# Kernel optimization log

Hardware: AMD Instinct MI355X
Metric: run time of the kernel (lower is better)

The kernel has to match this reference:

```python
import jax, jax.numpy as jnp
import numpy as np

B, S, D = 2, 2048, 1024
H = 16
HD = D // H  # 64


def setup_inputs() -> dict:
    key = jax.random.key(0)
    k1, k2, k3, k4, k5, k6 = jax.random.split(key, 6)
    hidden_states = jax.random.normal(k1, (B, S, D), dtype=jnp.float32)
    attention_mask = jax.random.randint(k2, (B, S), 0, 2, dtype=jnp.int32)
    scale = 1.0 / np.sqrt(D)
    Wq = jax.random.normal(k3, (D, D), dtype=jnp.float32) * scale
    bq = jax.random.normal(k4, (D,), dtype=jnp.float32) * 0.02
    Wk = jax.random.normal(k5, (D, D), dtype=jnp.float32) * scale
    bk = jax.random.normal(k6, (D,), dtype=jnp.float32) * 0.02
    return {"hidden_states": hidden_states, "attention_mask": attention_mask,
            "Wq": Wq, "bq": bq, "Wk": Wk, "bk": bk}


def _split_heads(x):
    # [B, S, D] -> [B, H, S, HD]
    b, s, _ = x.shape
    return x.reshape(b, s, H, HD).transpose(0, 2, 1, 3)


def reference(hidden_states, attention_mask, Wq, bq, Wk, bk):
    dh = jnp.sqrt(jnp.float32(HD))
    q = _split_heads(hidden_states @ Wq + bq)            # [B,H,S,HD]
    k = _split_heads(hidden_states @ Wk + bk)            # [B,H,S,HD]
    v = q + k                                            # value = Q + K
    k_t = -jax.nn.log_sigmoid(-k)                        # negate the logsigmoid(-K) transform
    scores = jnp.einsum('bhqd,bhkd->bhqk', q, k_t) / dh  # [B,H,S,S]
    # mask applied on the QUERY axis (dim 2), broadcast over key axis (faithful to source)
    mask = (attention_mask[:, None, :, None] == 0)       # [B,1,S,1]
    scores = jnp.where(mask, jnp.float32(-10000.0), scores)
    probs = jax.nn.softmax(scores, axis=-1)              # dropout: eval mode (identity)
    ctx = jnp.einsum('bhqk,bhkd->bhqd', probs, v)        # [B,H,S,HD]
    ctx = ctx.transpose(0, 2, 1, 3).reshape(B, S, D)
    return ctx
```

## Files before the change

### kernel.cpp

```cpp
#include <hip/hip_runtime.h>
#include <hip/hip_bf16.h>

#define B_ 2
#define S_ 2048
#define D_ 1024
#define H_ 16
#define HD_ 64

typedef __attribute__((ext_vector_type(8))) short short8;
typedef __attribute__((ext_vector_type(4))) short short4v;
typedef __attribute__((ext_vector_type(4))) float float4v;

typedef const __attribute__((address_space(1))) void* gas_ptr;
typedef __attribute__((address_space(3))) void* las_ptr;

static __device__ inline void gl_lds16(const void* g, void* l) {
  __builtin_amdgcn_global_load_lds((gas_ptr)g, (las_ptr)l, 16, 0, 0);
}

static __device__ inline short f2bs(float x) {
  __hip_bfloat16 h = __float2bfloat16(x);
  union { __hip_bfloat16 h; short s; } u; u.h = h; return u.s;
}
static __device__ inline float bs2f(short s) {
  union { short s; __hip_bfloat16 h; } u; u.s = s; return __bfloat162float(u.h);
}
static __device__ inline short4v pk4(float a, float b, float c, float d) {
  union { __hip_bfloat162 h[2]; short4v s; } u;
  u.h[0] = __float22bfloat162_rn(float2{a, b});
  u.h[1] = __float22bfloat162_rn(float2{c, d});
  return u.s;
}

static __device__ inline float4v mfma32(short8 a, short8 b, float4v c) {
  return __builtin_amdgcn_mfma_f32_16x16x32_bf16(a, b, c, 0, 0, 0);
}
static __device__ inline float4v mfma16(short4v a, short4v b, float4v c) {
  return __builtin_amdgcn_mfma_f32_16x16x16bf16_1k(a, b, c, 0, 0, 0);
}

__global__ __launch_bounds__(256) void prep(
    const float* __restrict__ hs, __hip_bfloat16* __restrict__ hsb,
    const float* __restrict__ Wq, const float* __restrict__ Wk,
    __hip_bfloat16* __restrict__ Wqt, __hip_bfloat16* __restrict__ Wkt) {
  __shared__ float t[64][65];
  const int id = blockIdx.x;
  if (id < 2048) {
    const size_t i = ((size_t)id * 256 + threadIdx.x) * 8;
    const float4v a0 = ((const float4v*)(hs + i))[0];
    const float4v a1 = ((const float4v*)(hs + i))[1];
    short8 s;
#pragma unroll
    for (int j = 0; j < 4; ++j) { s[j] = f2bs(a0[j]); s[4 + j] = f2bs(a1[j]); }
    *(short8*)(hsb + i) = s;
    return;
  }
  const int bid = id - 2048;
  const float* W = (bid >> 8) ? Wk : Wq;
  __hip_bfloat16* Wt = (bid >> 8) ? Wkt : Wqt;
  const int n0 = (bid & 15) * 64, k0 = ((bid >> 4) & 15) * 64;
  const int c = threadIdx.x & 63, r0 = threadIdx.x >> 6;
  for (int i = 0; i < 16; ++i) {
    const int r = i * 4 + r0;
    t[c][r] = W[(size_t)(k0 + r) * D_ + n0 + c];
  }
  __syncthreads();
  for (int i = 0; i < 16; ++i) {
    const int rr = i * 4 + r0;
    Wt[(size_t)(n0 + rr) * D_ + k0 + c] = __float2bfloat16(t[rr][c]);
  }
}

__global__ __launch_bounds__(256, 2) void gemm_fused(
    const __hip_bfloat16* __restrict__ hsb,
    const __hip_bfloat16* __restrict__ Wqt, const __hip_bfloat16* __restrict__ Wkt,
    const float* __restrict__ bq, const float* __restrict__ bk,
    __hip_bfloat16* __restrict__ q_out, __hip_bfloat16* __restrict__ kt_out,
    __hip_bfloat16* __restrict__ vT) {
  const int id = blockIdx.x;
  const int mt = (id & 7) * 8 + ((id >> 3) & 7);
  const int nt = id >> 6;
  const int n0 = nt * 128, m0 = mt * 64;
  __shared__ __hip_bfloat16 As[2][64 * 32];
  __shared__ __hip_bfloat16 Bq[2][128 * 32];
  __shared__ __hip_bfloat16 Bk[2][128 * 32];
  const int tid = threadIdx.x, wid = tid >> 6, lane = tid & 63;
  const int wm = (wid >> 1) * 32, wn = (wid & 1) * 64;
  const int l15 = lane & 15, l4 = lane >> 4;
  const float4v zz = {0.f, 0.f, 0.f, 0.f};
  float4v accq[2][4], acck[2][4];
  for (int i = 0; i < 2; ++i)
    for (int j = 0; j < 4; ++j) { accq[i][j] = zz; acck[i][j] = zz; }
  const int lrow = wid * 16 + (lane >> 2);
  const int lk8 = (((lane & 3) ^ ((lane >> 3) & 3)) * 8);
  {
    gl_lds16(hsb + (size_t)(m0 + lrow) * D_ + lk8, As[0] + wid * 512);
    gl_lds16(Wqt + (size_t)(n0 + lrow) * D_ + lk8, Bq[0] + wid * 512);
    gl_lds16(Wqt + (size_t)(n0 + 64 + lrow) * D_ + lk8, Bq[0] + 2048 + wid * 512);
    gl_lds16(Wkt + (size_t)(n0 + lrow) * D_ + lk8, Bk[0] + wid * 512);
    gl_lds16(Wkt + (size_t)(n0 + 64 + lrow) * D_ + lk8, Bk[0] + 2048 + wid * 512);
  }
  int p = 0;
  for (int kb = 0; kb < 32; ++kb) {
    __syncthreads();
    if (kb < 31) {
      const int kc = (kb + 1) * 32 + lk8;
      gl_lds16(hsb + (size_t)(m0 + lrow) * D_ + kc, As[p ^ 1] + wid * 512);
      gl_lds16(Wqt + (size_t)(n0 + lrow) * D_ + kc, Bq[p ^ 1] + wid * 512);
      gl_lds16(Wqt + (size_t)(n0 + 64 + lrow) * D_ + kc, Bq[p ^ 1] + 2048 + wid * 512);
      gl_lds16(Wkt + (size_t)(n0 + lrow) * D_ + kc, Bk[p ^ 1] + wid * 512);
      gl_lds16(Wkt + (size_t)(n0 + 64 + lrow) * D_ + kc, Bk[p ^ 1] + 2048 + wid * 512);
    }
    short8 af[2], bfq[4], bfk[4];
    const int fo = ((l4 ^ ((l15 >> 1) & 3)) * 8);
    for (int rt = 0; rt < 2; ++rt)
      af[rt] = *(const short8*)(As[p] + (wm + rt * 16 + l15) * 32 + fo);
    for (int ct = 0; ct < 4; ++ct) {
      bfq[ct] = *(const short8*)(Bq[p] + (wn + ct * 16 + l15) * 32 + fo);
      bfk[ct] = *(const short8*)(Bk[p] + (wn + ct * 16 + l15) * 32 + fo);
    }
    for (int rt = 0; rt < 2; ++rt)
      for (int ct = 0; ct < 4; ++ct) {
        accq[rt][ct] = mfma32(af[rt], bfq[ct], accq[rt][ct]);
        acck[rt][ct] = mfma32(af[rt], bfk[ct], acck[rt][ct]);
      }
    p ^= 1;
  }
  float bvq[4], bvk[4];
  for (int ct = 0; ct < 4; ++ct) {
    bvq[ct] = bq[n0 + wn + ct * 16 + l15];
    bvk[ct] = bk[n0 + wn + ct * 16 + l15];
  }
  for (int rt = 0; rt < 2; ++rt)
    for (int ct = 0; ct < 4; ++ct) {
      const int col = n0 + wn + ct * 16 + l15;
      const int h = col >> 6, d = col & 63;
      const int rowb = m0 + wm + rt * 16 + l4 * 4;
      short4v vv;
      for (int r = 0; r < 4; ++r) {
        const int row = rowb + r;
        const float qv = accq[rt][ct][r] + bvq[ct];
        const float kv = acck[rt][ct][r] + bvk[ct];
        const float sp = fmaxf(kv, 0.f) + __logf(1.f + __expf(-fabsf(kv)));
        q_out[(size_t)row * D_ + col] = __float2bfloat16(qv);
        kt_out[(size_t)row * D_ + col] = __float2bfloat16(sp);
        vv[r] = f2bs(qv + kv);
      }
      const int b = rowb >> 11, s = rowb & 2047;
      const int sw = (s & ~63) | (((s >> 4) & 3) << 2) | (((s >> 2) & 3) << 4);
      *(short4v*)(vT + ((size_t)(b * H_ + h) * HD_ + d) * S_ + sw) = vv;
    }
}

__global__ __launch_bounds__(256, 2) void attn(
    const __hip_bfloat16* __restrict__ qb, const __hip_bfloat16* __restrict__ ktb,
    const __hip_bfloat16* __restrict__ vT, const int* __restrict__ mask,
    float* __restrict__ out) {
  __shared__ short smem[32768];
  const int id = blockIdx.x;
  const int xcd = id & 7;
  const int rest = id >> 3;
  const int q0 = (rest & 15) * 128;
  const int hb = (rest >> 4) * 8 + xcd;
  const int h = hb >> 1, b = hb & 1;
  const int tid = threadIdx.x, wid = tid >> 6, lane = tid & 63;
  const int l15 = lane & 15, l4 = lane >> 4;
  const __hip_bfloat16* qh = qb + (size_t)b * S_ * D_ + h * HD_;
  const __hip_bfloat16* kh = ktb + (size_t)b * S_ * D_ + h * HD_;
  const __hip_bfloat16* vh = vT + (size_t)(b * H_ + h) * HD_ * S_;
  const int srow = tid >> 2;
  const int b0 = tid & 3;
  const int ssw = ((srow & 1) << 2) | ((srow >> 1) & 3);
  const int w0 = srow * 64 + ((b0 ^ ssw) * 8);
  const int w1 = srow * 64 + (((b0 + 4) ^ ssw) * 8);

  const int qlA = wid * 32 + l15, qlB = qlA + 16;
  const int qrA = q0 + qlA, qrB = q0 + qlB;
  const float SC = 0.125f * 1.44269504f;
  const float mqA = (mask[b * S_ + qrA] != 0) ? SC : 0.f;
  const float mqB = (mask[b * S_ + qrB] != 0) ? SC : 0.f;
  const short8 rA0 = *(const short8*)(qh + (size_t)qrA * D_ + l4 * 8);
  const short8 rA1 = *(const short8*)(qh + (size_t)qrA * D_ + 32 + l4 * 8);
  const short8 rB0 = *(const short8*)(qh + (size_t)qrB * D_ + l4 * 8);
  const short8 rB1 = *(const short8*)(qh + (size_t)qrB * D_ + 32 + l4 * 8);
  short8 bqA0, bqA1, bqB0, bqB1;
  for (int j = 0; j < 8; ++j) {
    bqA0[j] = f2bs(bs2f(rA0[j]) * mqA);
    bqA1[j] = f2bs(bs2f(rA1[j]) * mqA);
    bqB0[j] = f2bs(bs2f(rB0[j]) * mqB);
    bqB1[j] = f2bs(bs2f(rB1[j]) * mqB);
  }

  const int lsw = ((l15 & 1) << 2) | ((l15 >> 1) & 3);
  const int ak0off = l15 * 64 + ((l4 ^ lsw) * 8);
  const int ak1off = l15 * 64 + (((l4 + 4) ^ lsw) * 8);
  const int vb0off = ((2 * l4) ^ lsw) * 8;
  const int vb1off = ((2 * l4 + 1) ^ lsw) * 8;

  const float4v zz = {0.f, 0.f, 0.f, 0.f};
  float4v oaccA[4] = {zz, zz, zz, zz};
  float4v oaccB[4] = {zz, zz, zz, zz};
  float lsumA = 0.f, lsumB = 0.f;

  short8 gk0[2], gk1[2], gv0[2], gv1[2];
#pragma unroll
  for (int u = 0; u < 2; ++u) {
    gk0[u] = *(const short8*)(kh + (size_t)(u * 64 + srow) * D_ + b0 * 8);
    gk1[u] = *(const short8*)(kh + (size_t)(u * 64 + srow) * D_ + b0 * 8 + 32);
    gv0[u] = *(const short8*)(vh + (size_t)srow * S_ + u * 64 + b0 * 8);
    gv1[u] = *(const short8*)(vh + (size_t)srow * S_ + u * 64 + b0 * 8 + 32);
  }

  int p = 0;
  for (int c = 0; c < 16; ++c) {
    short* bufp = smem + p * 16384;
#pragma unroll
    for (int u = 0; u < 2; ++u) {
      *(short8*)(bufp + u * 4096 + w0) = gk0[u];
      *(short8*)(bufp + u * 4096 + w1) = gk1[u];
      *(short8*)(bufp + 8192 + u * 4096 + w0) = gv0[u];
      *(short8*)(bufp + 8192 + u * 4096 + w1) = gv1[u];
    }
    __syncthreads();
    if (c < 15) {
      const int kb = (c + 1) * 128;
#pragma unroll
      for (int u = 0; u < 2; ++u) {
        gk0[u] = *(const short8*)(kh + (size_t)(kb + u * 64 + srow) * D_ + b0 * 8);
        gk1[u] = *(const short8*)(kh + (size_t)(kb + u * 64 + srow) * D_ + b0 * 8 + 32);
        gv0[u] = *(const short8*)(vh + (size_t)srow * S_ + kb + u * 64 + b0 * 8);
        gv1[u] = *(const short8*)(vh + (size_t)srow * S_ + kb + u * 64 + b0 * 8 + 32);
      }
    }
#pragma unroll
    for (int u = 0; u < 2; ++u) {
      const short* kbase = bufp + u * 4096;
      const short* vbase = bufp + 8192 + u * 4096;
      short4v pA[4], pB[4];
#pragma unroll
      for (int t = 0; t < 4; ++t) {
        const short8 ak0 = *(const short8*)(kbase + t * 1024 + ak0off);
        const short8 ak1 = *(const short8*)(kbase + t * 1024 + ak1off);
        float4v cA = zz, cB = zz;
        cA = mfma32(ak0, bqA0, cA);
        cA = mfma32(ak1, bqA1, cA);
        cB = mfma32(ak0, bqB0, cB);
        cB = mfma32(ak1, bqB1, cB);
        float eA[4], eB[4];
#pragma unroll
        for (int r = 0; r < 4; ++r) {
          eA[r] = __builtin_amdgcn_exp2f(cA[r]); lsumA += eA[r];
          eB[r] = __builtin_amdgcn_exp2f(cB[r]); lsumB += eB[r];
        }
        pA[t] = pk4(eA[0], eA[1], eA[2], eA[3]);
        pB[t] = pk4(eB[0], eB[1], eB[2], eB[3]);
      }
#pragma unroll
      for (int dt = 0; dt < 4; ++dt) {
        const int rb = (dt * 16 + l15) * 64;
        const short8 av0 = *(const short8*)(vbase + rb + vb0off);
        const short8 av1 = *(const short8*)(vbase + rb + vb1off);
        const short4v a0 = {av0[0], av0[1], av0[2], av0[3]};
        const short4v a1 = {av0[4], av0[5], av0[6], av0[7]};
        const short4v a2 = {av1[0], av1[1], av1[2], av1[3]};
        const short4v a3 = {av1[4], av1[5], av1[6], av1[7]};
        oaccA[dt] = mfma16(a0, pA[0], oaccA[dt]);
        oaccB[dt] = mfma16(a0, pB[0], oaccB[dt]);
        oaccA[dt] = mfma16(a1, pA[1], oaccA[dt]);
        oaccB[dt] = mfma16(a1, pB[1], oaccB[dt]);
        oaccA[dt] = mfma16(a2, pA[2], oaccA[dt]);
        oaccB[dt] = mfma16(a2, pB[2], oaccB[dt]);
        oaccA[dt] = mfma16(a3, pA[3], oaccA[dt]);
        oaccB[dt] = mfma16(a3, pB[3], oaccB[dt]);
      }
    }
    p ^= 1;
  }
  float lA = lsumA + __shfl_xor(lsumA, 16); lA += __shfl_xor(lA, 32);
  float lB = lsumB + __shfl_xor(lsumB, 16); lB += __shfl_xor(lB, 32);
  __syncthreads();
  float* mbuf = (float*)smem;
  float* mlb = (float*)smem + 128 * 68;
#pragma unroll
  for (int dt = 0; dt < 4; ++dt)
#pragma unroll
    for (int r = 0; r < 4; ++r) {
      mbuf[qlA * 68 + dt * 16 + l4 * 4 + r] = oaccA[dt][r];
      mbuf[qlB * 68 + dt * 16 + l4 * 4 + r] = oaccB[dt][r];
    }
  if (l4 == 0) { mlb[qlA] = lA; mlb[qlB] = lB; }
  __syncthreads();
  const int qq = tid >> 1;
  const int dg = (tid & 1) * 32;
  const float li = 1.f / mlb[qq];
  float* orow = out + (size_t)(b * S_ + q0 + qq) * D_ + h * HD_ + dg;
#pragma unroll
  for (int i = 0; i < 8; ++i) {
    float4v v = *(const float4v*)&mbuf[qq * 68 + dg + i * 4];
#pragma unroll
    for (int r = 0; r < 4; ++r) v[r] *= li;
    *(float4v*)(orow + i * 4) = v;
  }
}

extern "C" void kernel_launch(void* const* d_in, const int* in_sizes, int n_in,
                              void* d_out, int out_size, void* d_ws, size_t ws_size,
                              hipStream_t stream) {
  const float* hs = (const float*)d_in[0];
  const int* mask = (const int*)d_in[1];
  const float* Wq = (const float*)d_in[2];
  const float* bq = (const float*)d_in[3];
  const float* Wk = (const float*)d_in[4];
  const float* bk = (const float*)d_in[5];
  float* out = (float*)d_out;
  char* ws = (char*)d_ws;
  const size_t MB = 1u << 20;
  __hip_bfloat16* q_b = (__hip_bfloat16*)(ws + 0 * MB);
  __hip_bfloat16* k_b = (__hip_bfloat16*)(ws + 8 * MB);
  __hip_bfloat16* vT  = (__hip_bfloat16*)(ws + 16 * MB);
  __hip_bfloat16* Wqt = (__hip_bfloat16*)(ws + 24 * MB);
  __hip_bfloat16* Wkt = (__hip_bfloat16*)(ws + 26 * MB);
  __hip_bfloat16* hsb = (__hip_bfloat16*)(ws + 28 * MB);

  prep<<<dim3(2560), 256, 0, stream>>>(hs, hsb, Wq, Wk, Wqt, Wkt);
  gemm_fused<<<dim3(512), 256, 0, stream>>>(hsb, Wqt, Wkt, bq, bk, q_b, k_b, vT);
  attn<<<dim3(512), 256, 0, stream>>>(q_b, k_b, vT, mask, out);
}
```

Before: 158.6 us.

## Double GEMM K-tile depth to 64 and vectorize attention epilogue stores

```diff
diff --git a/kernel.cpp b/kernel.cpp
--- a/kernel.cpp
+++ b/kernel.cpp
@@ -81,9 +81,9 @@
   const int mt = (id & 7) * 8 + ((id >> 3) & 7);
   const int nt = id >> 6;
   const int n0 = nt * 128, m0 = mt * 64;
-  __shared__ __hip_bfloat16 As[2][64 * 32];
-  __shared__ __hip_bfloat16 Bq[2][128 * 32];
-  __shared__ __hip_bfloat16 Bk[2][128 * 32];
+  __shared__ __hip_bfloat16 As[2][64 * 64];
+  __shared__ __hip_bfloat16 Bq[2][128 * 64];
+  __shared__ __hip_bfloat16 Bk[2][128 * 64];
   const int tid = threadIdx.x, wid = tid >> 6, lane = tid & 63;
   const int wm = (wid >> 1) * 32, wn = (wid & 1) * 64;
   const int l15 = lane & 15, l4 = lane >> 4;
@@ -91,41 +91,52 @@
   float4v accq[2][4], acck[2][4];
   for (int i = 0; i < 2; ++i)
     for (int j = 0; j < 4; ++j) { accq[i][j] = zz; acck[i][j] = zz; }
-  const int lrow = wid * 16 + (lane >> 2);
-  const int lk8 = (((lane & 3) ^ ((lane >> 3) & 3)) * 8);
-  {
-    gl_lds16(hsb + (size_t)(m0 + lrow) * D_ + lk8, As[0] + wid * 512);
-    gl_lds16(Wqt + (size_t)(n0 + lrow) * D_ + lk8, Bq[0] + wid * 512);
-    gl_lds16(Wqt + (size_t)(n0 + 64 + lrow) * D_ + lk8, Bq[0] + 2048 + wid * 512);
-    gl_lds16(Wkt + (size_t)(n0 + lrow) * D_ + lk8, Bk[0] + wid * 512);
-    gl_lds16(Wkt + (size_t)(n0 + 64 + lrow) * D_ + lk8, Bk[0] + 2048 + wid * 512);
-  }
+  const int srow8 = lane >> 3;
+  const int schunk = ((lane & 7) ^ (srow8 & 7)) * 8;
+  const int arow = wid * 16 + srow8;
+  const int brow = wid * 32 + srow8;
+#define STAGE(pp, kc)                                                          \
+  {                                                                            \
+    _Pragma("unroll")                                                          \
+    for (int j = 0; j < 2; ++j)                                                \
+      gl_lds16(hsb + (size_t)(m0 + arow + j * 8) * D_ + (kc) + schunk,         \
+               As[pp] + wid * 1024 + j * 512);                                 \
+    _Pragma("unroll")                                                          \
+    for (int j = 0; j < 4; ++j) {                                              \
+      gl_lds16(Wqt + (size_t)(n0 + brow + j * 8) * D_ + (kc) + schunk,         \
+               Bq[pp] + wid * 2048 + j * 512);                                 \
+      gl_lds16(Wkt + (size_t)(n0 + brow + j * 8) * D_ + (kc) + schunk,         \
+               Bk[pp] + wid * 2048 + j * 512);                                 \
+    }                                                                          \
+  }
+  STAGE(0, 0);
   int p = 0;
-  for (int kb = 0; kb < 32; ++kb) {
+  for (int kb = 0; kb < 16; ++kb) {
     __syncthreads();
-    if (kb < 31) {
-      const int kc = (kb + 1) * 32 + lk8;
-      gl_lds16(hsb + (size_t)(m0 + lrow) * D_ + kc, As[p ^ 1] + wid * 512);
-      gl_lds16(Wqt + (size_t)(n0 + lrow) * D_ + kc, Bq[p ^ 1] + wid * 512);
-      gl_lds16(Wqt + (size_t)(n0 + 64 + lrow) * D_ + kc, Bq[p ^ 1] + 2048 + wid * 512);
-      gl_lds16(Wkt + (size_t)(n0 + lrow) * D_ + kc, Bk[p ^ 1] + wid * 512);
-      gl_lds16(Wkt + (size_t)(n0 + 64 + lrow) * D_ + kc, Bk[p ^ 1] + 2048 + wid * 512);
-    }
-    short8 af[2], bfq[4], bfk[4];
-    const int fo = ((l4 ^ ((l15 >> 1) & 3)) * 8);
-    for (int rt = 0; rt < 2; ++rt)
-      af[rt] = *(const short8*)(As[p] + (wm + rt * 16 + l15) * 32 + fo);
-    for (int ct = 0; ct < 4; ++ct) {
-      bfq[ct] = *(const short8*)(Bq[p] + (wn + ct * 16 + l15) * 32 + fo);
-      bfk[ct] = *(const short8*)(Bk[p] + (wn + ct * 16 + l15) * 32 + fo);
-    }
-    for (int rt = 0; rt < 2; ++rt)
+    if (kb < 15) STAGE(p ^ 1, (kb + 1) * 64);
+#pragma unroll
+    for (int sub = 0; sub < 2; ++sub) {
+      short8 af[2], bfq[4], bfk[4];
+      const int fo = ((sub * 4 + l4) ^ (l15 & 7)) * 8;
+#pragma unroll
+      for (int rt = 0; rt < 2; ++rt)
+        af[rt] = *(const short8*)(As[p] + (wm + rt * 16 + l15) * 64 + fo);
+#pragma unroll
       for (int ct = 0; ct < 4; ++ct) {
-        accq[rt][ct] = mfma32(af[rt], bfq[ct], accq[rt][ct]);
-        acck[rt][ct] = mfma32(af[rt], bfk[ct], acck[rt][ct]);
-      }
+        bfq[ct] = *(const short8*)(Bq[p] + (wn + ct * 16 + l15) * 64 + fo);
+        bfk[ct] = *(const short8*)(Bk[p] + (wn + ct * 16 + l15) * 64 + fo);
+      }
+#pragma unroll
+      for (int rt = 0; rt < 2; ++rt)
+#pragma unroll
+        for (int ct = 0; ct < 4; ++ct) {
+          accq[rt][ct] = mfma32(af[rt], bfq[ct], accq[rt][ct]);
+          acck[rt][ct] = mfma32(af[rt], bfk[ct], acck[rt][ct]);
+        }
+    }
     p ^= 1;
   }
+#undef STAGE
   float bvq[4], bvk[4];
   for (int ct = 0; ct < 4; ++ct) {
     bvq[ct] = bq[n0 + wn + ct * 16 + l15];
@@ -200,7 +211,7 @@
   const float4v zz = {0.f, 0.f, 0.f, 0.f};
   float4v oaccA[4] = {zz, zz, zz, zz};
   float4v oaccB[4] = {zz, zz, zz, zz};
-  float lsumA = 0.f, lsumB = 0.f;
+  float4v lsA = zz, lsB = zz;
 
   short8 gk0[2], gk1[2], gv0[2], gv1[2];
 #pragma unroll
@@ -249,8 +260,8 @@
         float eA[4], eB[4];
 #pragma unroll
         for (int r = 0; r < 4; ++r) {
-          eA[r] = __builtin_amdgcn_exp2f(cA[r]); lsumA += eA[r];
-          eB[r] = __builtin_amdgcn_exp2f(cB[r]); lsumB += eB[r];
+          eA[r] = __builtin_amdgcn_exp2f(cA[r]); lsA[r] += eA[r];
+          eB[r] = __builtin_amdgcn_exp2f(cB[r]); lsB[r] += eB[r];
         }
         pA[t] = pk4(eA[0], eA[1], eA[2], eA[3]);
         pB[t] = pk4(eB[0], eB[1], eB[2], eB[3]);
@@ -276,22 +287,22 @@
     }
     p ^= 1;
   }
-  float lA = lsumA + __shfl_xor(lsumA, 16); lA += __shfl_xor(lA, 32);
-  float lB = lsumB + __shfl_xor(lsumB, 16); lB += __shfl_xor(lB, 32);
+  float lA = (lsA[0] + lsA[1]) + (lsA[2] + lsA[3]);
+  float lB = (lsB[0] + lsB[1]) + (lsB[2] + lsB[3]);
+  lA += __shfl_xor(lA, 16); lA += __shfl_xor(lA, 32);
+  lB += __shfl_xor(lB, 16); lB += __shfl_xor(lB, 32);
   __syncthreads();
   float* mbuf = (float*)smem;
   float* mlb = (float*)smem + 128 * 68;
 #pragma unroll
-  for (int dt = 0; dt < 4; ++dt)
-#pragma unroll
-    for (int r = 0; r < 4; ++r) {
-      mbuf[qlA * 68 + dt * 16 + l4 * 4 + r] = oaccA[dt][r];
-      mbuf[qlB * 68 + dt * 16 + l4 * 4 + r] = oaccB[dt][r];
-    }
+  for (int dt = 0; dt < 4; ++dt) {
+    *(float4v*)&mbuf[qlA * 68 + dt * 16 + l4 * 4] = oaccA[dt];
+    *(float4v*)&mbuf[qlB * 68 + dt * 16 + l4 * 4] = oaccB[dt];
+  }
   if (l4 == 0) { mlb[qlA] = lA; mlb[qlB] = lB; }
   __syncthreads();
-  const int qq = tid >> 1;
-  const int dg = (tid & 1) * 32;
+  const int qq = tid & 127;
+  const int dg = (tid >> 7) * 32;
   const float li = 1.f / mlb[qq];
   float* orow = out + (size_t)(b * S_ + q0 + qq) * D_ + h * HD_ + dg;
 #pragma unroll
```

New measurement: 160.2 us. No clear change (+1.0%).

## Split attention work across waves by query half and key half, reduce in LDS

Applied to the files above, without the earlier changes.

```diff
diff --git a/kernel.cpp b/kernel.cpp
--- a/kernel.cpp
+++ b/kernel.cpp
@@ -165,8 +165,10 @@
   const int h = hb >> 1, b = hb & 1;
   const int tid = threadIdx.x, wid = tid >> 6, lane = tid & 63;
   const int l15 = lane & 15, l4 = lane >> 4;
+  const int qs = (wid & 1) * 64;
+  const int kh = wid >> 1;
   const __hip_bfloat16* qh = qb + (size_t)b * S_ * D_ + h * HD_;
-  const __hip_bfloat16* kh = ktb + (size_t)b * S_ * D_ + h * HD_;
+  const __hip_bfloat16* kh_ = ktb + (size_t)b * S_ * D_ + h * HD_;
   const __hip_bfloat16* vh = vT + (size_t)(b * H_ + h) * HD_ * S_;
   const int srow = tid >> 2;
   const int b0 = tid & 3;
@@ -174,21 +176,19 @@
   const int w0 = srow * 64 + ((b0 ^ ssw) * 8);
   const int w1 = srow * 64 + (((b0 + 4) ^ ssw) * 8);
 
-  const int qlA = wid * 32 + l15, qlB = qlA + 16;
-  const int qrA = q0 + qlA, qrB = q0 + qlB;
   const float SC = 0.125f * 1.44269504f;
-  const float mqA = (mask[b * S_ + qrA] != 0) ? SC : 0.f;
-  const float mqB = (mask[b * S_ + qrB] != 0) ? SC : 0.f;
-  const short8 rA0 = *(const short8*)(qh + (size_t)qrA * D_ + l4 * 8);
-  const short8 rA1 = *(const short8*)(qh + (size_t)qrA * D_ + 32 + l4 * 8);
-  const short8 rB0 = *(const short8*)(qh + (size_t)qrB * D_ + l4 * 8);
-  const short8 rB1 = *(const short8*)(qh + (size_t)qrB * D_ + 32 + l4 * 8);
-  short8 bqA0, bqA1, bqB0, bqB1;
-  for (int j = 0; j < 8; ++j) {
-    bqA0[j] = f2bs(bs2f(rA0[j]) * mqA);
-    bqA1[j] = f2bs(bs2f(rA1[j]) * mqA);
-    bqB0[j] = f2bs(bs2f(rB0[j]) * mqB);
-    bqB1[j] = f2bs(bs2f(rB1[j]) * mqB);
+  short8 bq0[4], bq1[4];
+#pragma unroll
+  for (int T = 0; T < 4; ++T) {
+    const int qr = q0 + qs + T * 16 + l15;
+    const float mq = (mask[b * S_ + qr] != 0) ? SC : 0.f;
+    const short8 r0 = *(const short8*)(qh + (size_t)qr * D_ + l4 * 8);
+    const short8 r1 = *(const short8*)(qh + (size_t)qr * D_ + 32 + l4 * 8);
+#pragma unroll
+    for (int j = 0; j < 8; ++j) {
+      bq0[T][j] = f2bs(bs2f(r0[j]) * mq);
+      bq1[T][j] = f2bs(bs2f(r1[j]) * mq);
+    }
   }
 
   const int lsw = ((l15 & 1) << 2) | ((l15 >> 1) & 3);
@@ -198,22 +198,25 @@
   const int vb1off = ((2 * l4 + 1) ^ lsw) * 8;
 
   const float4v zz = {0.f, 0.f, 0.f, 0.f};
-  float4v oaccA[4] = {zz, zz, zz, zz};
-  float4v oaccB[4] = {zz, zz, zz, zz};
-  float lsumA = 0.f, lsumB = 0.f;
+  float4v oacc[4][4];
+#pragma unroll
+  for (int T = 0; T < 4; ++T)
+#pragma unroll
+    for (int dt = 0; dt < 4; ++dt) oacc[T][dt] = zz;
+  float4v ls[4] = {zz, zz, zz, zz};
 
   short8 gk0[2], gk1[2], gv0[2], gv1[2];
 #pragma unroll
   for (int u = 0; u < 2; ++u) {
-    gk0[u] = *(const short8*)(kh + (size_t)(u * 64 + srow) * D_ + b0 * 8);
-    gk1[u] = *(const short8*)(kh + (size_t)(u * 64 + srow) * D_ + b0 * 8 + 32);
+    gk0[u] = *(const short8*)(kh_ + (size_t)(u * 64 + srow) * D_ + b0 * 8);
+    gk1[u] = *(const short8*)(kh_ + (size_t)(u * 64 + srow) * D_ + b0 * 8 + 32);
     gv0[u] = *(const short8*)(vh + (size_t)srow * S_ + u * 64 + b0 * 8);
     gv1[u] = *(const short8*)(vh + (size_t)srow * S_ + u * 64 + b0 * 8 + 32);
   }
 
-  int p = 0;
+  int pb = 0;
   for (int c = 0; c < 16; ++c) {
-    short* bufp = smem + p * 16384;
+    short* bufp = smem + pb * 16384;
 #pragma unroll
     for (int u = 0; u < 2; ++u) {
       *(short8*)(bufp + u * 4096 + w0) = gk0[u];
@@ -226,72 +229,88 @@
       const int kb = (c + 1) * 128;
 #pragma unroll
       for (int u = 0; u < 2; ++u) {
-        gk0[u] = *(const short8*)(kh + (size_t)(kb + u * 64 + srow) * D_ + b0 * 8);
-        gk1[u] = *(const short8*)(kh + (size_t)(kb + u * 64 + srow) * D_ + b0 * 8 + 32);
+        gk0[u] = *(const short8*)(kh_ + (size_t)(kb + u * 64 + srow) * D_ + b0 * 8);
+        gk1[u] = *(const short8*)(kh_ + (size_t)(kb + u * 64 + srow) * D_ + b0 * 8 + 32);
         gv0[u] = *(const short8*)(vh + (size_t)srow * S_ + kb + u * 64 + b0 * 8);
         gv1[u] = *(const short8*)(vh + (size_t)srow * S_ + kb + u * 64 + b0 * 8 + 32);
       }
     }
-#pragma unroll
-    for (int u = 0; u < 2; ++u) {
-      const short* kbase = bufp + u * 4096;
-      const short* vbase = bufp + 8192 + u * 4096;
-      short4v pA[4], pB[4];
-#pragma unroll
-      for (int t = 0; t < 4; ++t) {
-        const short8 ak0 = *(const short8*)(kbase + t * 1024 + ak0off);
-        const short8 ak1 = *(const short8*)(kbase + t * 1024 + ak1off);
-        float4v cA = zz, cB = zz;
-        cA = mfma32(ak0, bqA0, cA);
-        cA = mfma32(ak1, bqA1, cA);
-        cB = mfma32(ak0, bqB0, cB);
-        cB = mfma32(ak1, bqB1, cB);
-        float eA[4], eB[4];
+    const short* kbase = bufp + kh * 4096;
+    const short* vbase = bufp + 8192 + kh * 4096;
+    short4v pf[4][4];
+#pragma unroll
+    for (int t = 0; t < 4; ++t) {
+      const short8 ak0 = *(const short8*)(kbase + t * 1024 + ak0off);
+      const short8 ak1 = *(const short8*)(kbase + t * 1024 + ak1off);
+#pragma unroll
+      for (int T = 0; T < 4; ++T) {
+        float4v cc = zz;
+        cc = mfma32(ak0, bq0[T], cc);
+        cc = mfma32(ak1, bq1[T], cc);
+        float e[4];
 #pragma unroll
         for (int r = 0; r < 4; ++r) {
-          eA[r] = __builtin_amdgcn_exp2f(cA[r]); lsumA += eA[r];
-          eB[r] = __builtin_amdgcn_exp2f(cB[r]); lsumB += eB[r];
+          e[r] = __builtin_amdgcn_exp2f(cc[r]); ls[T][r] += e[r];
         }
-        pA[t] = pk4(eA[0], eA[1], eA[2], eA[3]);
-        pB[t] = pk4(eB[0], eB[1], eB[2], eB[3]);
-      }
-#pragma unroll
-      for (int dt = 0; dt < 4; ++dt) {
-        const int rb = (dt * 16 + l15) * 64;
-        const short8 av0 = *(const short8*)(vbase + rb + vb0off);
-        const short8 av1 = *(const short8*)(vbase + rb + vb1off);
-        const short4v a0 = {av0[0], av0[1], av0[2], av0[3]};
-        const short4v a1 = {av0[4], av0[5], av0[6], av0[7]};
-        const short4v a2 = {av1[0], av1[1], av1[2], av1[3]};
-        const short4v a3 = {av1[4], av1[5], av1[6], av1[7]};
-        oaccA[dt] = mfma16(a0, pA[0], oaccA[dt]);
-        oaccB[dt] = mfma16(a0, pB[0], oaccB[dt]);
-        oaccA[dt] = mfma16(a1, pA[1], oaccA[dt]);
-        oaccB[dt] = mfma16(a1, pB[1], oaccB[dt]);
-        oaccA[dt] = mfma16(a2, pA[2], oaccA[dt]);
-        oaccB[dt] = mfma16(a2, pB[2], oaccB[dt]);
-        oaccA[dt] = mfma16(a3, pA[3], oaccA[dt]);
-        oaccB[dt] = mfma16(a3, pB[3], oaccB[dt]);
-      }
-    }
-    p ^= 1;
-  }
-  float lA = lsumA + __shfl_xor(lsumA, 16); lA += __shfl_xor(lA, 32);
-  float lB = lsumB + __shfl_xor(lsumB, 16); lB += __shfl_xor(lB, 32);
+        pf[T][t] = pk4(e[0], e[1], e[2], e[3]);
+      }
+    }
+#pragma unroll
+    for (int dt = 0; dt < 4; ++dt) {
+      const int rb = (dt * 16 + l15) * 64;
+      const short8 av0 = *(const short8*)(vbase + rb + vb0off);
+      const short8 av1 = *(const short8*)(vbase + rb + vb1off);
+      const short4v a0 = {av0[0], av0[1], av0[2], av0[3]};
+      const short4v a1 = {av0[4], av0[5], av0[6], av0[7]};
+      const short4v a2 = {av1[0], av1[1], av1[2], av1[3]};
+      const short4v a3 = {av1[4], av1[5], av1[6], av1[7]};
+#pragma unroll
+      for (int T = 0; T < 4; ++T) {
+        oacc[T][dt] = mfma16(a0, pf[T][0], oacc[T][dt]);
+        oacc[T][dt] = mfma16(a1, pf[T][1], oacc[T][dt]);
+        oacc[T][dt] = mfma16(a2, pf[T][2], oacc[T][dt]);
+        oacc[T][dt] = mfma16(a3, pf[T][3], oacc[T][dt]);
+      }
+    }
+    pb ^= 1;
+  }
+  float lT[4];
+#pragma unroll
+  for (int T = 0; T < 4; ++T) {
+    lT[T] = (ls[T][0] + ls[T][1]) + (ls[T][2] + ls[T][3]);
+    lT[T] += __shfl_xor(lT[T], 16);
+    lT[T] += __shfl_xor(lT[T], 32);
+  }
   __syncthreads();
   float* mbuf = (float*)smem;
   float* mlb = (float*)smem + 128 * 68;
-#pragma unroll
-  for (int dt = 0; dt < 4; ++dt)
-#pragma unroll
-    for (int r = 0; r < 4; ++r) {
-      mbuf[qlA * 68 + dt * 16 + l4 * 4 + r] = oaccA[dt][r];
-      mbuf[qlB * 68 + dt * 16 + l4 * 4 + r] = oaccB[dt][r];
-    }
-  if (l4 == 0) { mlb[qlA] = lA; mlb[qlB] = lB; }
+  if (kh == 0) {
+#pragma unroll
+    for (int T = 0; T < 4; ++T) {
+      const int row = qs + T * 16 + l15;
+#pragma unroll
+      for (int dt = 0; dt < 4; ++dt)
+        *(float4v*)&mbuf[row * 68 + dt * 16 + l4 * 4] = oacc[T][dt];
+      if (l4 == 0) mlb[row] = lT[T];
+    }
+  }
   __syncthreads();
-  const int qq = tid >> 1;
-  const int dg = (tid & 1) * 32;
+  if (kh == 1) {
+#pragma unroll
+    for (int T = 0; T < 4; ++T) {
+      const int row = qs + T * 16 + l15;
+#pragma unroll
+      for (int dt = 0; dt < 4; ++dt) {
+        float4v v = *(const float4v*)&mbuf[row * 68 + dt * 16 + l4 * 4];
+        v += oacc[T][dt];
+        *(float4v*)&mbuf[row * 68 + dt * 16 + l4 * 4] = v;
+      }
+      if (l4 == 0) mlb[row] += lT[T];
+    }
+  }
+  __syncthreads();
+  const int qq = tid & 127;
+  const int dg = (tid >> 7) * 32;
   const float li = 1.f / mlb[qq];
   float* orow = out + (size_t)(b * S_ + q0 + qq) * D_ + h * HD_ + dg;
 #pragma unroll
```

New measurement: 158.1 us. Within noise of the previous version (-0.3%).
